# Optimization experiments

Hardware: AMD Instinct MI355X
Metric: run time of the kernel (lower is better)

The kernel has to match this reference:

```python
import jax, jax.numpy as jnp
import numpy as np
import math

B, S, E = 4, 2048, 1024
H, D = 16, 64

def setup_inputs() -> dict:
    key = jax.random.key(0)
    ks = jax.random.split(key, 9)
    s = 0.02
    return {
        "x":  jax.random.normal(ks[0], (B, S, E), dtype=jnp.float32),
        "Wq": jax.random.normal(ks[1], (H, E, D), dtype=jnp.float32) * s,
        "Wk": jax.random.normal(ks[2], (H, E, D), dtype=jnp.float32) * s,
        "Wv": jax.random.normal(ks[3], (H, E, D), dtype=jnp.float32) * s,
        "bq": jax.random.normal(ks[4], (H, D), dtype=jnp.float32) * s,
        "bk": jax.random.normal(ks[5], (H, D), dtype=jnp.float32) * s,
        "bv": jax.random.normal(ks[6], (H, D), dtype=jnp.float32) * s,
        "Wo": jax.random.normal(ks[7], (H * D, E), dtype=jnp.float32) * s,
        "bo": jax.random.normal(ks[8], (E,), dtype=jnp.float32) * s,
    }

def reference(x, Wq, Wk, Wv, bq, bk, bv, Wo, bo):
    # batched per-head projections: [B,S,E] x [H,E,D] -> [B,H,S,D]
    Q = jnp.einsum('bse,hed->bhsd', x, Wq) + bq[None, :, None, :]
    K = jnp.einsum('bse,hed->bhsd', x, Wk) + bk[None, :, None, :]
    V = jnp.einsum('bse,hed->bhsd', x, Wv) + bv[None, :, None, :]
    scale = 1.0 / math.sqrt(D)
    scores = jnp.einsum('bhqd,bhkd->bhqk', Q, K) * scale  # [B,H,S,S]
    causal = jnp.tril(jnp.ones((S, S), dtype=bool))
    scores = jnp.where(causal, scores, -jnp.inf)
    attn = jax.nn.softmax(scores, axis=-1)
    ctx = jnp.einsum('bhqk,bhkd->bhqd', attn, V)  # [B,H,S,D]
    # concat heads along last dim == transpose to [B,S,H,D] then reshape
    conc = ctx.transpose(0, 2, 1, 3).reshape(B, S, H * D)
    out = conc @ Wo + bo  # dropout is identity in eval
    return out
```

## Files before the change

kernel.cpp:

```cpp
#include <hip/hip_runtime.h>
#include <stdint.h>

#define Bn 4
#define Sn 2048
#define En 1024
#define Hn 16
#define Dn 64

#define QSC 0.18033688011112f

typedef unsigned short u16;
typedef short s16x8 __attribute__((ext_vector_type(8)));
typedef float f32x4 __attribute__((ext_vector_type(4)));

#define MFMA16x16x32 __builtin_amdgcn_mfma_f32_16x16x32_bf16

__device__ __forceinline__ u16 f2bf(float f) {
  union { float f; uint32_t u; } v; v.f = f;
  uint32_t u = v.u;
  u += 0x7fffu + ((u >> 16) & 1u);
  return (u16)(u >> 16);
}
__device__ __forceinline__ uint32_t f2u(float f) {
  union { float f; uint32_t u; } v; v.f = f; return v.u;
}

#define AS1 __attribute__((address_space(1)))
#define AS3 __attribute__((address_space(3)))
__device__ __forceinline__ void gload_lds16(const void* g, void* l) {
  __builtin_amdgcn_global_load_lds((const AS1 uint32_t*)g, (AS3 uint32_t*)l, 16, 0, 0);
}

__global__ __launch_bounds__(256) void prep_all(
    const float4* __restrict__ x4, ushort4* __restrict__ xb4,
    const float* __restrict__ Wq, const float* __restrict__ Wk,
    const float* __restrict__ Wv, u16* __restrict__ WallT,
    const float* __restrict__ Wo, u16* __restrict__ WoT,
    const float* __restrict__ bq, const float* __restrict__ bk,
    const float* __restrict__ bv, float* __restrict__ biasA)
{
  __shared__ float t[64][65];
  const int tid = threadIdx.x;
  int blk = blockIdx.x;

  if (blk < 8192) {
    int i = blk * 256 + tid;
    float4 v = x4[i];
    ushort4 o;
    o.x = f2bf(v.x); o.y = f2bf(v.y); o.z = f2bf(v.z); o.w = f2bf(v.w);
    xb4[i] = o;
    return;
  }
  blk -= 8192;
  if (blk < 768) {
    const int e0 = (blk & 15) * 64;
    const int sh = blk >> 4;
    const int sec = sh >> 4, h = sh & 15;
    const float* W = (sec == 0) ? Wq : (sec == 1) ? Wk : Wv;
    const float* Wh = W + (size_t)h * En * Dn;
    const int d = tid & 63, er = tid >> 6;
#pragma unroll
    for (int ee = 0; ee < 64; ee += 4)
      t[ee + er][d] = Wh[(size_t)(e0 + ee + er) * Dn + d];
    __syncthreads();
    const int dd = tid >> 2, eo = (tid & 3) * 16;
    u16* dst = WallT + (size_t)(sec * 1024 + h * 64 + dd) * En + e0 + eo;
#pragma unroll
    for (int i = 0; i < 16; i += 4) {
      ushort4 o;
      o.x = f2bf(t[eo + i + 0][dd]);
      o.y = f2bf(t[eo + i + 1][dd]);
      o.z = f2bf(t[eo + i + 2][dd]);
      o.w = f2bf(t[eo + i + 3][dd]);
      *(ushort4*)(dst + i) = o;
    }
    return;
  }
  blk -= 768;
  if (blk < 256) {
    const int k0 = (blk & 15) * 64;
    const int n0 = (blk >> 4) * 64;
    const int c = tid & 63, r4 = tid >> 6;
#pragma unroll
    for (int rr = 0; rr < 64; rr += 4)
      t[rr + r4][c] = Wo[(size_t)(k0 + rr + r4) * En + n0 + c];
    __syncthreads();
    const int n = tid >> 2, ko = (tid & 3) * 16;
    u16* dst = WoT + (size_t)(n0 + n) * (Hn * Dn) + k0 + ko;
#pragma unroll
    for (int i = 0; i < 16; i += 4) {
      ushort4 o;
      o.x = f2bf(t[ko + i + 0][n]);
      o.y = f2bf(t[ko + i + 1][n]);
      o.z = f2bf(t[ko + i + 2][n]);
      o.w = f2bf(t[ko + i + 3][n]);
      *(ushort4*)(dst + i) = o;
    }
    return;
  }
  blk -= 256;
  int n = blk * 256 + tid;
  if (n < 3 * Hn * Dn) {
    int sec = n >> 10, rr = n & 1023;
    const float* bs = (sec == 0) ? bq : (sec == 1) ? bk : bv;
    biasA[n] = bs[rr];
  }
}

template<int MODE>
__global__ __launch_bounds__(256) void gemm_bt(
    const u16* __restrict__ A, const u16* __restrict__ Bt,
    const float* __restrict__ bias, int M, int N, int K,
    u16* __restrict__ q_out, u16* __restrict__ k_out, u16* __restrict__ v_out,
    float* __restrict__ f_out)
{
  extern __shared__ __align__(16) u16 smem[];

  const int tid  = threadIdx.x;
  const int L    = blockIdx.x;
  const int m0   = (L & 63) * 128;
  const int n0   = (L >> 6) * 128;
  const int w    = tid >> 6;
  const int lane = tid & 63;
  const int quad = lane >> 4;
  const int l15  = lane & 15;
  const int mbase = (w >> 1) * 64;
  const int nbase = (w & 1) * 64;
  const int swz   = (quad ^ ((l15 >> 1) & 3)) * 8;

  f32x4 acc[4][4];
#pragma unroll
  for (int i = 0; i < 4; ++i)
#pragma unroll
    for (int j = 0; j < 4; ++j)
      acc[i][j] = (f32x4){0.f, 0.f, 0.f, 0.f};

  auto stage = [&](int k0, int bf) {
    u16* lA = smem + bf * 4096;
    u16* lB = smem + 2 * 4096 + bf * 4096;
#pragma unroll
    for (int c = 0; c < 2; ++c) {
      int idx = c * 256 + tid;
      int row = idx >> 2, sl = idx & 3;
      int sg = sl ^ ((row >> 1) & 3);
      gload_lds16(A  + (size_t)(m0 + row) * K + k0 + sg * 8, &lA[idx * 8]);
      gload_lds16(Bt + (size_t)(n0 + row) * K + k0 + sg * 8, &lB[idx * 8]);
    }
  };

  stage(0, 0);
  int bf = 0;
  for (int k0 = 0; k0 < K; k0 += 32) {
    __syncthreads();
    if (k0 + 32 < K) stage(k0 + 32, bf ^ 1);
    const u16* lA = smem + bf * 4096;
    const u16* lB = smem + 2 * 4096 + bf * 4096;

    s16x8 af[4], bfr[4];
#pragma unroll
    for (int t = 0; t < 4; ++t) {
      af[t]  = *(const s16x8*)&lA[(mbase + t * 16 + l15) * 32 + swz];
      bfr[t] = *(const s16x8*)&lB[(nbase + t * 16 + l15) * 32 + swz];
    }
#pragma unroll
    for (int mt = 0; mt < 4; ++mt)
#pragma unroll
      for (int nt = 0; nt < 4; ++nt)
        acc[mt][nt] = MFMA16x16x32(af[mt], bfr[nt], acc[mt][nt], 0, 0, 0);
    bf ^= 1;
  }

  {
#pragma unroll
    for (int nt = 0; nt < 4; ++nt) {
      int col = n0 + nbase + nt * 16 + l15;
      float bv = bias[col];
#pragma unroll
      for (int mt = 0; mt < 4; ++mt)
#pragma unroll
        for (int r = 0; r < 4; ++r) {
          int row = m0 + mbase + mt * 16 + quad * 4 + r;
          f_out[(size_t)row * N + col] = acc[mt][nt][r] + bv;
        }
    }
  }
}

__global__ __launch_bounds__(256, 3) void gemm_qkv2(
    const u16* __restrict__ A, const u16* __restrict__ Bt,
    const float* __restrict__ bias,
    u16* __restrict__ q_out, u16* __restrict__ k_out, u16* __restrict__ v_out)
{
  extern __shared__ __align__(16) u16 smem[];

  const int tid  = threadIdx.x;
  const int L    = blockIdx.x;
  const int xcd  = L & 7;
  const int rl   = L >> 3;
  const int mi   = rl / 3;
  const int ni   = xcd * 3 + (rl - mi * 3);
  const int m0   = mi * 256;
  const int n0   = ni * 128;

  const int w    = tid >> 6;
  const int lane = tid & 63;
  const int quad = lane >> 4;
  const int l15  = lane & 15;
  const int wm   = w >> 1;
  const int wn   = w & 1;
  const int swz  = (quad ^ ((l15 >> 1) & 3)) * 8;

  f32x4 acc[8][4];
#pragma unroll
  for (int i = 0; i < 8; ++i)
#pragma unroll
    for (int j = 0; j < 4; ++j)
      acc[i][j] = (f32x4){0.f, 0.f, 0.f, 0.f};

  auto stage = [&](int t) {
    const int db = t & 1;
    const int k0 = t * 32;
    u16* lA = smem + db * 8192;
    u16* lB = smem + 16384 + db * 4096;
#pragma unroll
    for (int c = 0; c < 4; ++c) {
      int idx = c * 256 + tid;
      int row = idx >> 2, sl = idx & 3;
      int sg = sl ^ ((row >> 1) & 3);
      gload_lds16(A + (size_t)(m0 + row) * En + k0 + sg * 8, &lA[idx * 8]);
    }
#pragma unroll
    for (int c = 0; c < 2; ++c) {
      int idx = c * 256 + tid;
      int row = idx >> 2, sl = idx & 3;
      int sg = sl ^ ((row >> 1) & 3);
      gload_lds16(Bt + (size_t)(n0 + row) * En + k0 + sg * 8, &lB[idx * 8]);
    }
  };

  stage(0);
  for (int t = 0; t < 32; ++t) {
    __syncthreads();
    if (t + 1 < 32) stage(t + 1);
    const u16* cA = smem + (t & 1) * 8192;
    const u16* cB = smem + 16384 + (t & 1) * 4096;

    s16x8 bf4[4];
#pragma unroll
    for (int nt = 0; nt < 4; ++nt)
      bf4[nt] = *(const s16x8*)&cB[(wn * 64 + nt * 16 + l15) * 32 + swz];
#pragma unroll
    for (int mt = 0; mt < 8; ++mt) {
      s16x8 af = *(const s16x8*)&cA[(wm * 128 + mt * 16 + l15) * 32 + swz];
#pragma unroll
      for (int nt = 0; nt < 4; ++nt)
        acc[mt][nt] = MFMA16x16x32(af, bf4[nt], acc[mt][nt], 0, 0, 0);
    }
  }

  const int sec = n0 >> 10;
  if (sec < 2) {
    const float osc = (sec == 0) ? QSC : 1.0f;
    u16* dst = (sec == 0) ? q_out : k_out;
#pragma unroll
    for (int nt = 0; nt < 4; ++nt) {
      int col = n0 + wn * 64 + nt * 16 + l15;
      float bv = bias[col];
      int rr = col & 1023;
      int h = rr >> 6, d = rr & 63;
#pragma unroll
      for (int mt = 0; mt < 8; ++mt)
#pragma unroll
        for (int r = 0; r < 4; ++r) {
          int row = m0 + wm * 128 + mt * 16 + quad * 4 + r;
          int b = row >> 11, s = row & 2047;
          dst[(((size_t)b * Hn + h) * Sn + s) * Dn + d] =
              f2bf((acc[mt][nt][r] + bv) * osc);
        }
    }
  } else {
    __syncthreads();
    u16* lC = smem;
    const int b = m0 >> 11;
#pragma unroll
    for (int p = 0; p < 2; ++p) {
      if (wm == p) {
#pragma unroll
        for (int nt = 0; nt < 4; ++nt) {
          int cl = wn * 64 + nt * 16 + l15;
          float bv = bias[n0 + cl];
#pragma unroll
          for (int mt = 0; mt < 8; ++mt)
#pragma unroll
            for (int r = 0; r < 4; ++r)
              lC[cl * 136 + mt * 16 + quad * 4 + r] = f2bf(acc[mt][nt][r] + bv);
        }
      }
      __syncthreads();
      int c = tid >> 1, hh = tid & 1;
      int colg = (n0 & 1023) + c;
      int h = colg >> 6, d = colg & 63;
      int s0 = (m0 & 2047) + p * 128 + hh * 64;
      const uint4* src = (const uint4*)&lC[c * 136 + hh * 64];
      uint4* dstv = (uint4*)&v_out[(((size_t)b * Hn + h) * Dn + d) * Sn + s0];
#pragma unroll
      for (int i = 0; i < 8; ++i) dstv[i] = src[i];
      if (p == 0) __syncthreads();
    }
  }
}

__global__ __launch_bounds__(256, 4) void flash_attn(
    const u16* __restrict__ Qb, const u16* __restrict__ Kb,
    const u16* __restrict__ Vt, u16* __restrict__ conc)
{
  __shared__ __align__(16) u16 lK[2][64 * 64];
  __shared__ __align__(16) u16 lV[2][64 * 64];
  __shared__ __align__(16) u16 lP[4][16 * 64];

  const int L   = blockIdx.x;
  const int bh  = L & 63;
  const int qt  = ((L >> 6) + (bh >> 2)) & 15;
  const int b   = bh >> 4, h = bh & 15;
  const int tid = threadIdx.x;
  const int w   = tid >> 6;
  const int lane = tid & 63;
  const int quad = lane >> 4;
  const int l15  = lane & 15;
  const int q0   = qt * 128;

  const u16* Qh = Qb + (size_t)bh * Sn * Dn;
  const u16* Kh = Kb + (size_t)bh * Sn * Dn;
  const u16* Vh = Vt + (size_t)bh * Dn * Sn;

  const int Q0m[2] = { q0 + w * 16, q0 + 64 + w * 16 };

  s16x8 aq[2][2];
#pragma unroll
  for (int m = 0; m < 2; ++m)
#pragma unroll
    for (int c = 0; c < 2; ++c)
      aq[m][c] = *(const s16x8*)&Qh[(size_t)(Q0m[m] + l15) * Dn + c * 32 + quad * 8];

  s16x8 kones;
#pragma unroll
  for (int i = 0; i < 8; ++i) kones[i] = (short)0x3F80;

  f32x4 acc[2][4];
#pragma unroll
  for (int m = 0; m < 2; ++m)
#pragma unroll
    for (int i = 0; i < 4; ++i) acc[m][i] = (f32x4){0.f, 0.f, 0.f, 0.f};
  const float NEG_INF = -__builtin_inff();
  float lrow[2] = {0.f, 0.f};

  const int sw0 = (quad ^ (l15 & 7)) * 8;
  const int sw1 = ((quad + 4) ^ (l15 & 7)) * 8;
  const int l7  = l15 & 7;

  const int ntiles = 2 * qt + 2;

  auto stage = [&](int kt) {
    int bufb = kt & 1;
    int kk0 = kt * 64;
#pragma unroll
    for (int c = 0; c < 2; ++c) {
      int idx = c * 256 + tid;
      int row = idx >> 3, sl = idx & 7;
      int sg = sl ^ (row & 7);
      gload_lds16(Kh + (size_t)(kk0 + row) * Dn + sg * 8, &lK[bufb][idx * 8]);
      gload_lds16(Vh + (size_t)row * Sn + kk0 + sg * 8, &lV[bufb][idx * 8]);
    }
  };

  stage(0);
  for (int kt = 0; kt < ntiles; ++kt) {
    const int kk0 = kt * 64;
    __syncthreads();
    if (kt + 1 < ntiles) stage(kt + 1);
    const u16* cK = lK[kt & 1];
    const u16* cV = lV[kt & 1];

#pragma unroll
    for (int m = 0; m < 2; ++m) {
      const int Q0 = Q0m[m];
      if (kk0 >= Q0 + 16) continue;

      f32x4 sc[4];
#pragma unroll
      for (int ct = 0; ct < 4; ++ct) {
        s16x8 bk0 = *(const s16x8*)&cK[(ct * 16 + l15) * 64 + sw0];
        s16x8 bk1 = *(const s16x8*)&cK[(ct * 16 + l15) * 64 + sw1];
        f32x4 z = (f32x4){0.f, 0.f, 0.f, 0.f};
        z = MFMA16x16x32(bk0, aq[m][0], z, 0, 0, 0);
        z = MFMA16x16x32(bk1, aq[m][1], z, 0, 0, 0);
        sc[ct] = z;
      }

      const int qg = Q0 + l15;
      if (kk0 + 63 > Q0) {
#pragma unroll
        for (int ct = 0; ct < 4; ++ct)
#pragma unroll
          for (int r = 0; r < 4; ++r) {
            int kkg = kk0 + ct * 16 + quad * 4 + r;
            sc[ct][r] = (kkg <= qg) ? sc[ct][r] : NEG_INF;
          }
      }

#pragma unroll
      for (int ct = 0; ct < 4; ++ct)
#pragma unroll
        for (int r = 0; r < 4; ++r)
          sc[ct][r] = __builtin_amdgcn_exp2f(sc[ct][r]);

      u16* Pw = &lP[w][0];
#pragma unroll
      for (int ct = 0; ct < 4; ++ct) {
        uint32_t d0 = __builtin_amdgcn_perm(f2u(sc[ct][1]), f2u(sc[ct][0]), 0x07060302);
        uint32_t d1 = __builtin_amdgcn_perm(f2u(sc[ct][3]), f2u(sc[ct][2]), 0x07060302);
        uint2 pk; pk.x = d0; pk.y = d1;
        int seg = (ct * 2 + (quad >> 1)) ^ l7;
        *(uint2*)&Pw[l15 * 64 + seg * 8 + (quad & 1) * 4] = pk;
      }
      __builtin_amdgcn_s_waitcnt(0xc07f);

      s16x8 ap0 = *(const s16x8*)&Pw[l15 * 64 + (quad ^ l7) * 8];
      s16x8 ap1 = *(const s16x8*)&Pw[l15 * 64 + ((quad + 4) ^ l7) * 8];

      f32x4 zl = (f32x4){0.f, 0.f, 0.f, 0.f};
      zl = MFMA16x16x32(kones, ap0, zl, 0, 0, 0);
      zl = MFMA16x16x32(kones, ap1, zl, 0, 0, 0);

#pragma unroll
      for (int dt = 0; dt < 4; ++dt) {
        s16x8 bv0 = *(const s16x8*)&cV[(dt * 16 + l15) * 64 + sw0];
        s16x8 bv1 = *(const s16x8*)&cV[(dt * 16 + l15) * 64 + sw1];
        acc[m][dt] = MFMA16x16x32(bv0, ap0, acc[m][dt], 0, 0, 0);
        acc[m][dt] = MFMA16x16x32(bv1, ap1, acc[m][dt], 0, 0, 0);
      }
      lrow[m] += zl[0];
    }
  }

#pragma unroll
  for (int m = 0; m < 2; ++m) {
    float inv = 1.0f / lrow[m];
    int qg = Q0m[m] + l15;
#pragma unroll
    for (int dt = 0; dt < 4; ++dt) {
      ushort4 o;
      o.x = f2bf(acc[m][dt][0] * inv);
      o.y = f2bf(acc[m][dt][1] * inv);
      o.z = f2bf(acc[m][dt][2] * inv);
      o.w = f2bf(acc[m][dt][3] * inv);
      *(ushort4*)&conc[((size_t)b * Sn + qg) * (Hn * Dn) + h * Dn + dt * 16 + quad * 4] = o;
    }
  }
}

extern "C" void kernel_launch(void* const* d_in, const int* in_sizes, int n_in,
                              void* d_out, int out_size, void* d_ws, size_t ws_size,
                              hipStream_t stream)
{
  const float* x  = (const float*)d_in[0];
  const float* Wq = (const float*)d_in[1];
  const float* Wk = (const float*)d_in[2];
  const float* Wv = (const float*)d_in[3];
  const float* bq = (const float*)d_in[4];
  const float* bk = (const float*)d_in[5];
  const float* bv = (const float*)d_in[6];
  const float* Wo = (const float*)d_in[7];
  const float* bo = (const float*)d_in[8];
  float* out = (float*)d_out;

  char* p = (char*)d_ws;
  u16* xb    = (u16*)p; p += (size_t)Bn * Sn * En * sizeof(u16);
  u16* WallT = (u16*)p; p += (size_t)3 * Hn * Dn * En * sizeof(u16);
  u16* WoT   = (u16*)p; p += (size_t)En * Hn * Dn * sizeof(u16);
  float* biasA = (float*)p; p += (size_t)3 * Hn * Dn * sizeof(float);
  u16* Qb    = (u16*)p; p += (size_t)Bn * Hn * Sn * Dn * sizeof(u16);
  u16* Kb    = (u16*)p; p += (size_t)Bn * Hn * Sn * Dn * sizeof(u16);
  u16* Vt    = (u16*)p; p += (size_t)Bn * Hn * Dn * Sn * sizeof(u16);
  u16* conc  = (u16*)p; p += (size_t)Bn * Sn * Hn * Dn * sizeof(u16);

  prep_all<<<9228, 256, 0, stream>>>((const float4*)x, (ushort4*)xb,
                                     Wq, Wk, Wv, WallT, Wo, WoT,
                                     bq, bk, bv, biasA);

  size_t smemq = 24576 * sizeof(u16);
  gemm_qkv2<<<768, 256, smemq, stream>>>(xb, WallT, biasA, Qb, Kb, Vt);

  flash_attn<<<(Sn / 128) * Bn * Hn, 256, 0, stream>>>(Qb, Kb, Vt, conc);

  size_t smem1 = 4 * 4096 * sizeof(u16);
  gemm_bt<1><<<8 * 64, 256, smem1, stream>>>(
      conc, WoT, bo, Bn * Sn, En, Hn * Dn, nullptr, nullptr, nullptr, out);
}
```

Baseline: 254.9 us.

## Rewrite QKV GEMM as 256x256 tile, 8-wave ping-pong pipelined kernel

Replaces the 256x128-tile, 4-wave QKV projection GEMM with a 256x256-tile, 8-wave kernel. It uses a K-step of 64, double-buffered 128KB LDS, and an interleaved schedule that issues global-to-LDS loads between MFMA quadrant groups. Barriers and explicit waitcnts order the stages, and s_setprio raises priority during MFMA bursts. The aim is more data reuse per tile and better overlap of loads with compute. The cost is higher LDS use (one block per CU) and more intricate synchronization that is error-prone.

Measured after the change: 258.7 us. No clear change (+1.5%).

```diff
diff --git a/kernel.cpp b/kernel.cpp
--- a/kernel.cpp
+++ b/kernel.cpp
@@ -186,29 +186,87 @@
   }
 }
 
-__global__ __launch_bounds__(256, 3) void gemm_qkv2(
+#define QBAR __builtin_amdgcn_s_barrier()
+#define QWL  asm volatile("s_waitcnt lgkmcnt(0)" ::: "memory")
+
+#define LDA8(DB, MQ)                                                           \
+  do {                                                                         \
+    const u16* p_ = smem + (DB) * 16384 + wm * 8192;                           \
+    _Pragma("unroll")                                                          \
+    for (int i_ = 0; i_ < 4; ++i_) {                                           \
+      const u16* r_ = p_ + ((MQ) * 64 + i_ * 16 + l15) * 64;                   \
+      af[i_][0] = *(const s16x8*)&r_[sw0];                                     \
+      af[i_][1] = *(const s16x8*)&r_[sw1];                                     \
+    }                                                                          \
+  } while (0)
+
+#define LDB8(DB, NQ, BF)                                                       \
+  do {                                                                         \
+    const u16* p_ = smem + 32768 + (DB) * 16384 + (wn >> 1) * 8192 +           \
+                    (wn & 1) * 4096;                                           \
+    _Pragma("unroll")                                                          \
+    for (int j_ = 0; j_ < 2; ++j_) {                                           \
+      const u16* r_ = p_ + ((NQ) * 32 + j_ * 16 + l15) * 64;                   \
+      BF[j_][0] = *(const s16x8*)&r_[sw0];                                     \
+      BF[j_][1] = *(const s16x8*)&r_[sw1];                                     \
+    }                                                                          \
+  } while (0)
+
+#define MM16(MQ, NQ, BF)                                                       \
+  do {                                                                         \
+    __builtin_amdgcn_s_setprio(1);                                             \
+    _Pragma("unroll")                                                          \
+    for (int i_ = 0; i_ < 4; ++i_)                                             \
+      _Pragma("unroll")                                                        \
+      for (int j_ = 0; j_ < 2; ++j_) {                                         \
+        acc[(MQ) * 4 + i_][(NQ) * 2 + j_] =                                    \
+            MFMA16x16x32(af[i_][0], BF[j_][0],                                 \
+                         acc[(MQ) * 4 + i_][(NQ) * 2 + j_], 0, 0, 0);          \
+        acc[(MQ) * 4 + i_][(NQ) * 2 + j_] =                                    \
+            MFMA16x16x32(af[i_][1], BF[j_][1],                                 \
+                         acc[(MQ) * 4 + i_][(NQ) * 2 + j_], 0, 0, 0);          \
+      }                                                                        \
+    __builtin_amdgcn_s_setprio(0);                                             \
+  } while (0)
+
+__global__ __launch_bounds__(512, 2) void gemm_qkv8(
     const u16* __restrict__ A, const u16* __restrict__ Bt,
     const float* __restrict__ bias,
     u16* __restrict__ q_out, u16* __restrict__ k_out, u16* __restrict__ v_out)
 {
   extern __shared__ __align__(16) u16 smem[];
 
-  const int tid  = threadIdx.x;
-  const int L    = blockIdx.x;
-  const int xcd  = L & 7;
-  const int rl   = L >> 3;
-  const int mi   = rl / 3;
-  const int ni   = xcd * 3 + (rl - mi * 3);
-  const int m0   = mi * 256;
-  const int n0   = ni * 128;
+  const int tid = threadIdx.x;
+  const int L   = blockIdx.x;
+  const int g   = (L & 7) * 48 + (L >> 3);
+  const int mi  = g / 12, ni = g - mi * 12;
+  const int m0  = mi * 256, n0 = ni * 256;
 
   const int w    = tid >> 6;
   const int lane = tid & 63;
   const int quad = lane >> 4;
   const int l15  = lane & 15;
-  const int wm   = w >> 1;
-  const int wn   = w & 1;
-  const int swz  = (quad ^ ((l15 >> 1) & 3)) * 8;
+  const int l7   = lane & 7;
+  const int wm   = w >> 2;
+  const int wn   = w & 3;
+  const int sw0  = (quad ^ l7) * 8;
+  const int sw1  = ((quad + 4) ^ l7) * 8;
+
+  const int srow = tid >> 3, ssl = tid & 7;
+  const int sseg = ssl ^ (srow & 7);
+
+  auto stA = [&](int kt, int db, int h) {
+    const u16* src = A + (size_t)(m0 + h * 128 + srow) * En + kt * 64 + sseg * 8;
+    u16* dst = smem + db * 16384 + h * 8192 + tid * 8;
+    gload_lds16(src, dst);
+    gload_lds16(src + (size_t)64 * En, dst + 4096);
+  };
+  auto stB = [&](int kt, int db, int h) {
+    const u16* src = Bt + (size_t)(n0 + h * 128 + srow) * En + kt * 64 + sseg * 8;
+    u16* dst = smem + 32768 + db * 16384 + h * 8192 + tid * 8;
+    gload_lds16(src, dst);
+    gload_lds16(src + (size_t)64 * En, dst + 4096);
+  };
 
   f32x4 acc[8][4];
 #pragma unroll
@@ -217,45 +275,47 @@
     for (int j = 0; j < 4; ++j)
       acc[i][j] = (f32x4){0.f, 0.f, 0.f, 0.f};
 
-  auto stage = [&](int t) {
-    const int db = t & 1;
-    const int k0 = t * 32;
-    u16* lA = smem + db * 8192;
-    u16* lB = smem + 16384 + db * 4096;
-#pragma unroll
-    for (int c = 0; c < 4; ++c) {
-      int idx = c * 256 + tid;
-      int row = idx >> 2, sl = idx & 3;
-      int sg = sl ^ ((row >> 1) & 3);
-      gload_lds16(A + (size_t)(m0 + row) * En + k0 + sg * 8, &lA[idx * 8]);
-    }
-#pragma unroll
-    for (int c = 0; c < 2; ++c) {
-      int idx = c * 256 + tid;
-      int row = idx >> 2, sl = idx & 3;
-      int sg = sl ^ ((row >> 1) & 3);
-      gload_lds16(Bt + (size_t)(n0 + row) * En + k0 + sg * 8, &lB[idx * 8]);
-    }
-  };
-
-  stage(0);
-  for (int t = 0; t < 32; ++t) {
-    __syncthreads();
-    if (t + 1 < 32) stage(t + 1);
-    const u16* cA = smem + (t & 1) * 8192;
-    const u16* cB = smem + 16384 + (t & 1) * 4096;
-
-    s16x8 bf4[4];
-#pragma unroll
-    for (int nt = 0; nt < 4; ++nt)
-      bf4[nt] = *(const s16x8*)&cB[(wn * 64 + nt * 16 + l15) * 32 + swz];
-#pragma unroll
-    for (int mt = 0; mt < 8; ++mt) {
-      s16x8 af = *(const s16x8*)&cA[(wm * 128 + mt * 16 + l15) * 32 + swz];
-#pragma unroll
-      for (int nt = 0; nt < 4; ++nt)
-        acc[mt][nt] = MFMA16x16x32(af, bf4[nt], acc[mt][nt], 0, 0, 0);
-    }
+  s16x8 af[4][2], bfa[2][2], bfb[2][2];
+
+  stA(0, 0, 0); stA(0, 0, 1); stB(0, 0, 0); stB(0, 0, 1);
+  stB(1, 1, 0); stB(1, 1, 1);
+  asm volatile("s_waitcnt vmcnt(4)" ::: "memory");
+  QBAR;
+
+  for (int it = 0; it < 8; ++it) {
+    const int t = 2 * it;
+    const int u = t + 1;
+    const bool st = (it < 7);
+
+    LDA8(0, 0); LDB8(0, 0, bfa);
+    stA(u, 1, 0);
+    QBAR; QWL; MM16(0, 0, bfa); QBAR;
+    LDB8(0, 1, bfb);
+    stA(u, 1, 1);
+    QBAR; QWL; MM16(0, 1, bfb); QBAR;
+    LDA8(0, 1);
+    if (st) stB(t + 2, 0, 0);
+    QBAR; QWL; MM16(1, 1, bfb); QBAR;
+    if (st) stB(t + 2, 0, 1);
+    QBAR; MM16(1, 0, bfa);
+    if (st) asm volatile("s_waitcnt vmcnt(4)" ::: "memory");
+    else    asm volatile("s_waitcnt vmcnt(0)" ::: "memory");
+    QBAR;
+
+    LDA8(1, 0); LDB8(1, 0, bfa);
+    if (st) stA(t + 2, 0, 0);
+    QBAR; QWL; MM16(0, 0, bfa); QBAR;
+    LDB8(1, 1, bfb);
+    if (st) stA(t + 2, 0, 1);
+    QBAR; QWL; MM16(0, 1, bfb); QBAR;
+    LDA8(1, 1);
+    if (st) stB(u + 2, 1, 0);
+    QBAR; QWL; MM16(1, 1, bfb); QBAR;
+    if (st) stB(u + 2, 1, 1);
+    QBAR; MM16(1, 0, bfa);
+    if (st) asm volatile("s_waitcnt vmcnt(4)" ::: "memory");
+    else    asm volatile("s_waitcnt vmcnt(0)" ::: "memory");
+    QBAR;
   }
 
   const int sec = n0 >> 10;
@@ -488,8 +548,7 @@
                                      Wq, Wk, Wv, WallT, Wo, WoT,
                                      bq, bk, bv, biasA);
 
-  size_t smemq = 24576 * sizeof(u16);
-  gemm_qkv2<<<768, 256, smemq, stream>>>(xb, WallT, biasA, Qb, Kb, Vt);
+  gemm_qkv8<<<384, 512, 131072, stream>>>(xb, WallT, biasA, Qb, Kb, Vt);
 
   flash_attn<<<(Sn / 128) * Bn * Hn, 256, 0, stream>>>(Qb, Kb, Vt, conc);
 
```
